# Performance work log

Measured on AMD Instinct MI355X. Metric: run time of the kernel, lower is better.

## Reference

```python
import jax, jax.numpy as jnp
import numpy as np
from jax import lax

MARGIN = 1.0
LAMDA = 0.003
EPS = 1e-9


def extract_features(f, idx):
    # f: (B,C,h,w); idx: (B,N,2) int with idx[...,0]=x, idx[...,1]=y -> (B*N, C)
    B, N = idx.shape[:2]
    b = jnp.arange(B)[:, None]
    x = idx[..., 0]
    y = idx[..., 1]
    g = f[b, :, y, x]  # (B, N, C)
    return g.reshape(B * N, f.shape[1])


def grad_axis(f, axis):
    # np.gradient along one axis: central differences, one-sided at edges
    fl = jnp.moveaxis(f, axis, 0)
    g = jnp.concatenate([
        fl[1:2] - fl[0:1],
        (fl[2:] - fl[:-2]) * 0.5,
        fl[-1:] - fl[-2:-1],
    ], axis=0)
    return jnp.moveaxis(g, 0, axis)


def contrastive(fa, fb, N, pos):
    diff = fa - fb
    if pos:
        return jnp.sum(diff * diff / N)
    m = jnp.maximum(MARGIN - diff, 0.0)
    return jnp.sum(m * m / N)


def gn_loss(f_t, fb, ub):
    # f_t: (B*N, C) target features; fb: (B,C,h,w); ub: (B,N,2) int matches
    B, N = ub.shape[:2]
    xs = ub  # deterministic stand-in for round(rand + ub) rejection sampling
    f_s = extract_features(fb, xs)
    r = f_s - f_t  # (BN, C)
    fbd = lax.stop_gradient(fb)  # original uses fb.detach() for gradients
    gy = grad_axis(fbd, 2)
    gx = grad_axis(fbd, 3)
    Jx = extract_features(gx, xs)  # (BN, C)
    Jy = extract_features(gy, xs)
    J = jnp.stack([Jx, Jy], axis=-1)  # (BN, C, 2)
    H = jnp.einsum('nci,ncj->nij', J, J) + EPS * jnp.eye(2, dtype=fb.dtype)
    b = jnp.einsum('nci,nc->ni', J, r)  # (BN, 2)
    xsf = xs.reshape(B * N, 2).astype(fb.dtype)
    miu = xsf - jnp.einsum('nij,nj->ni', jnp.linalg.inv(H), b)
    d = ub.reshape(B * N, 2).astype(fb.dtype) - miu
    e1 = 0.5 * jnp.sum(jnp.einsum('na,nab,nb->n', d, H, d))
    log_det = jnp.log(jnp.linalg.det(H))
    e2 = B * N * jnp.log(jnp.asarray(2.0 * np.pi, fb.dtype)) - 0.5 * jnp.sum(log_det)
    return e1 + e2


def gn_forward(F_a, F_b, ka, kb, na, nb):
    N = ka.shape[1]
    fa4 = extract_features(F_a[-1], ka)
    fb4 = extract_features(F_b[-1], kb)
    loss = 0.0
    for i in range(4):
        level = 2 ** (3 - i)
        if i == 3:
            fa_pos, fb_pos = fa4, fb4
        else:
            fa_pos = extract_features(F_a[i], ka // level)
            fb_pos = extract_features(F_b[i], kb // level)
        fa_neg = extract_features(F_a[i], na // level)
        fb_neg = extract_features(F_b[i], nb // level)
        loss_pos = contrastive(fa_pos, fb_pos, N, pos=True)
        loss_neg = contrastive(fa_neg, fb_neg, N, pos=False)
        loss_gn = gn_loss(fa_pos, F_b[i], kb // level)
        loss = loss_pos + loss_neg + LAMDA * loss_gn + loss
    return loss


def setup_inputs() -> dict:
    key = jax.random.key(0)
    ks = jax.random.split(key, 12)
    B, C, H, W, N = 4, 64, 256, 256, 512
    inp = {}
    for j, (name, s) in enumerate([
        ('fa0', 32), ('fa1', 64), ('fa2', 128), ('fa3', 256),
        ('fb0', 32), ('fb1', 64), ('fb2', 128), ('fb3', 256)]):
        inp[name] = jax.random.normal(ks[j], (B, C, s, s), dtype=jnp.float32)
    for j, name in enumerate(['ka', 'kb', 'na', 'nb']):
        inp[name] = jax.random.randint(ks[8 + j], (B, N, 2), 0, 256, dtype=jnp.int32)
    return inp


def reference(fa0, fa1, fa2, fa3, fb0, fb1, fb2, fb3, ka, kb, na, nb):
    F_a = [fa0, fa1, fa2, fa3]
    F_b = [fb0, fb1, fb2, fb3]
    return gn_forward(F_a, F_b, ka, kb, na, nb)
```

## Files before the change

### kernel.cpp

```cpp
#include <hip/hip_runtime.h>

#define MARGIN 1.0f
#define LAMDA  0.003f
#define EPS_H  1e-9f

#define E2_CONST (0.003f * 4.0f * 2048.0f * 1.8378770664093453f)

__global__ __launch_bounds__(256) void gn_task_kernel(
    const float* __restrict__ fa0, const float* __restrict__ fa1,
    const float* __restrict__ fa2, const float* __restrict__ fa3,
    const float* __restrict__ fb0, const float* __restrict__ fb1,
    const float* __restrict__ fb2, const float* __restrict__ fb3,
    const int* __restrict__ ka, const int* __restrict__ kb,
    const int* __restrict__ na, const int* __restrict__ nb,
    float* __restrict__ partial)
{
    const int wave = threadIdx.x >> 6;
    const int lane = threadIdx.x & 63;
    const int level = wave;
    const int n     = blockIdx.x;
    const int task  = level * 2048 + n;
    const int b     = n >> 9;
    const int shift = 3 - level;
    const int S     = 32 << level;

    const float* fa; const float* fb;
    switch (level) {
        case 0:  fa = fa0; fb = fb0; break;
        case 1:  fa = fa1; fb = fb1; break;
        case 2:  fa = fa2; fb = fb2; break;
        default: fa = fa3; fb = fb3; break;
    }

    const int pidx = n * 2;
    const int kax = ka[pidx]     >> shift;
    const int kay = ka[pidx + 1] >> shift;
    const int kbx = kb[pidx]     >> shift;
    const int kby = kb[pidx + 1] >> shift;
    const int nax = na[pidx]     >> shift;
    const int nay = na[pidx + 1] >> shift;
    const int nbx = nb[pidx]     >> shift;
    const int nby = nb[pidx + 1] >> shift;

    const int plane = (b * 64 + lane) * (S * S);

    const float va  = fa[plane + kay * S + kax];
    const float vb  = fb[plane + kby * S + kbx];
    const float vna = fa[plane + nay * S + nax];
    const float vnb = fb[plane + nby * S + nbx];

    const int   xm = (kbx > 0)     ? kbx - 1 : 0;
    const int   xp = (kbx < S - 1) ? kbx + 1 : S - 1;
    const float sx = (kbx > 0 && kbx < S - 1) ? 0.5f : 1.0f;
    const float Jx = (fb[plane + kby * S + xp] - fb[plane + kby * S + xm]) * sx;

    const int   ym = (kby > 0)     ? kby - 1 : 0;
    const int   yp = (kby < S - 1) ? kby + 1 : S - 1;
    const float sy = (kby > 0 && kby < S - 1) ? 0.5f : 1.0f;
    const float Jy = (fb[plane + yp * S + kbx] - fb[plane + ym * S + kbx]) * sy;

    const float dpos = va - vb;
    const float dneg = vna - vnb;
    const float mneg = fmaxf(MARGIN - dneg, 0.0f);
    const float r    = vb - va;

    float vals[7];
    vals[0] = dpos * dpos;
    vals[1] = mneg * mneg;
    vals[2] = Jx * Jx;
    vals[3] = Jx * Jy;
    vals[4] = Jy * Jy;
    vals[5] = Jx * r;
    vals[6] = Jy * r;

    #pragma unroll
    for (int mask = 32; mask >= 1; mask >>= 1) {
        #pragma unroll
        for (int t = 0; t < 7; ++t)
            vals[t] += __shfl_xor(vals[t], mask, 64);
    }

    if (lane == 0) {
        const float Hxx = vals[2] + EPS_H;
        const float Hxy = vals[3];
        const float Hyy = vals[4] + EPS_H;
        const float bX  = vals[5];
        const float bY  = vals[6];
        const float det = Hxx * Hyy - Hxy * Hxy;
        const float e1  = 0.5f * (Hyy * bX * bX - 2.0f * Hxy * bX * bY + Hxx * bY * bY) / det;
        const float out = (vals[0] + vals[1]) * (1.0f / 512.0f)
                        + LAMDA * (e1 - 0.5f * logf(det));
        partial[task] = out;
    }
}

__global__ __launch_bounds__(256) void gn_reduce_kernel(
    const float* __restrict__ partial, float* __restrict__ out)
{
    __shared__ float sm[256];
    float s = 0.0f;
    for (int i = threadIdx.x; i < 8192; i += 256)
        s += partial[i];
    sm[threadIdx.x] = s;
    __syncthreads();
    #pragma unroll
    for (int off = 128; off >= 1; off >>= 1) {
        if (threadIdx.x < off)
            sm[threadIdx.x] += sm[threadIdx.x + off];
        __syncthreads();
    }
    if (threadIdx.x == 0)
        out[0] = sm[0] + E2_CONST;
}

extern "C" void kernel_launch(void* const* d_in, const int* in_sizes, int n_in,
                              void* d_out, int out_size, void* d_ws, size_t ws_size,
                              hipStream_t stream) {
    const float* fa0 = (const float*)d_in[0];
    const float* fa1 = (const float*)d_in[1];
    const float* fa2 = (const float*)d_in[2];
    const float* fa3 = (const float*)d_in[3];
    const float* fb0 = (const float*)d_in[4];
    const float* fb1 = (const float*)d_in[5];
    const float* fb2 = (const float*)d_in[6];
    const float* fb3 = (const float*)d_in[7];
    const int*   ka  = (const int*)d_in[8];
    const int*   kb  = (const int*)d_in[9];
    const int*   na  = (const int*)d_in[10];
    const int*   nb  = (const int*)d_in[11];

    float* partial = (float*)d_ws;
    float* out     = (float*)d_out;

    gn_task_kernel<<<2048, 256, 0, stream>>>(fa0, fa1, fa2, fa3,
                                             fb0, fb1, fb2, fb3,
                                             ka, kb, na, nb, partial);
    gn_reduce_kernel<<<1, 256, 0, stream>>>(partial, out);
}
```

Before: 53.68 us.

## Process two points per wave and fuse final reduction via atomics

```diff
diff --git a/kernel.cpp b/kernel.cpp
--- a/kernel.cpp
+++ b/kernel.cpp
@@ -6,6 +6,43 @@
 
 #define E2_CONST (0.003f * 4.0f * 2048.0f * 1.8378770664093453f)
 
+struct PointVals { float v[7]; };
+
+__device__ __forceinline__ void point_addrs(
+    const int* __restrict__ ka, const int* __restrict__ kb,
+    const int* __restrict__ na, const int* __restrict__ nb,
+    int n, int shift, int S, int plane,
+    int& a_pos, int& a_neg_a, int& a_bpos, int& a_neg_b,
+    int& a_xm, int& a_xp, int& a_ym, int& a_yp,
+    float& sx, float& sy)
+{
+    const int2 kA = ((const int2*)ka)[n];
+    const int2 kB = ((const int2*)kb)[n];
+    const int2 nA = ((const int2*)na)[n];
+    const int2 nB = ((const int2*)nb)[n];
+    const int kax = kA.x >> shift, kay = kA.y >> shift;
+    const int kbx = kB.x >> shift, kby = kB.y >> shift;
+    const int nax = nA.x >> shift, nay = nA.y >> shift;
+    const int nbx = nB.x >> shift, nby = nB.y >> shift;
+
+    a_pos   = plane + kay * S + kax;
+    a_neg_a = plane + nay * S + nax;
+    a_bpos  = plane + kby * S + kbx;
+    a_neg_b = plane + nby * S + nbx;
+
+    const int xm = (kbx > 0)     ? kbx - 1 : 0;
+    const int xp = (kbx < S - 1) ? kbx + 1 : S - 1;
+    sx = (kbx > 0 && kbx < S - 1) ? 0.5f : 1.0f;
+    a_xm = plane + kby * S + xm;
+    a_xp = plane + kby * S + xp;
+
+    const int ym = (kby > 0)     ? kby - 1 : 0;
+    const int yp = (kby < S - 1) ? kby + 1 : S - 1;
+    sy = (kby > 0 && kby < S - 1) ? 0.5f : 1.0f;
+    a_ym = plane + ym * S + kbx;
+    a_yp = plane + yp * S + kbx;
+}
+
 __global__ __launch_bounds__(256) void gn_task_kernel(
     const float* __restrict__ fa0, const float* __restrict__ fa1,
     const float* __restrict__ fa2, const float* __restrict__ fa3,
@@ -13,16 +50,19 @@
     const float* __restrict__ fb2, const float* __restrict__ fb3,
     const int* __restrict__ ka, const int* __restrict__ kb,
     const int* __restrict__ na, const int* __restrict__ nb,
-    float* __restrict__ partial)
+    float* __restrict__ out)
 {
+    __shared__ float blk[4];
     const int wave = threadIdx.x >> 6;
     const int lane = threadIdx.x & 63;
     const int level = wave;
-    const int n     = blockIdx.x;
-    const int task  = level * 2048 + n;
-    const int b     = n >> 9;
     const int shift = 3 - level;
     const int S     = 32 << level;
+
+    const int n0 = blockIdx.x;
+    const int n1 = blockIdx.x + 1024;
+    const int b0 = n0 >> 9;
+    const int b1 = n1 >> 9;
 
     const float* fa; const float* fb;
     switch (level) {
@@ -32,85 +72,86 @@
         default: fa = fa3; fb = fb3; break;
     }
 
-    const int pidx = n * 2;
-    const int kax = ka[pidx]     >> shift;
-    const int kay = ka[pidx + 1] >> shift;
-    const int kbx = kb[pidx]     >> shift;
-    const int kby = kb[pidx + 1] >> shift;
-    const int nax = na[pidx]     >> shift;
-    const int nay = na[pidx + 1] >> shift;
-    const int nbx = nb[pidx]     >> shift;
-    const int nby = nb[pidx + 1] >> shift;
+    const int plane0 = (b0 * 64 + lane) * (S * S);
+    const int plane1 = (b1 * 64 + lane) * (S * S);
 
-    const int plane = (b * 64 + lane) * (S * S);
+    int p0_pos, p0_na, p0_bp, p0_nb, p0_xm, p0_xp, p0_ym, p0_yp;
+    int p1_pos, p1_na, p1_bp, p1_nb, p1_xm, p1_xp, p1_ym, p1_yp;
+    float sx0, sy0, sx1, sy1;
+    point_addrs(ka, kb, na, nb, n0, shift, S, plane0,
+                p0_pos, p0_na, p0_bp, p0_nb, p0_xm, p0_xp, p0_ym, p0_yp, sx0, sy0);
+    point_addrs(ka, kb, na, nb, n1, shift, S, plane1,
+                p1_pos, p1_na, p1_bp, p1_nb, p1_xm, p1_xp, p1_ym, p1_yp, sx1, sy1);
 
-    const float va  = fa[plane + kay * S + kax];
-    const float vb  = fb[plane + kby * S + kbx];
-    const float vna = fa[plane + nay * S + nax];
-    const float vnb = fb[plane + nby * S + nbx];
+    const float va0  = fa[p0_pos];
+    const float vna0 = fa[p0_na];
+    const float vb0  = fb[p0_bp];
+    const float vnb0 = fb[p0_nb];
+    const float gxm0 = fb[p0_xm];
+    const float gxp0 = fb[p0_xp];
+    const float gym0 = fb[p0_ym];
+    const float gyp0 = fb[p0_yp];
+    const float va1  = fa[p1_pos];
+    const float vna1 = fa[p1_na];
+    const float vb1  = fb[p1_bp];
+    const float vnb1 = fb[p1_nb];
+    const float gxm1 = fb[p1_xm];
+    const float gxp1 = fb[p1_xp];
+    const float gym1 = fb[p1_ym];
+    const float gyp1 = fb[p1_yp];
 
-    const int   xm = (kbx > 0)     ? kbx - 1 : 0;
-    const int   xp = (kbx < S - 1) ? kbx + 1 : S - 1;
-    const float sx = (kbx > 0 && kbx < S - 1) ? 0.5f : 1.0f;
-    const float Jx = (fb[plane + kby * S + xp] - fb[plane + kby * S + xm]) * sx;
+    const float Jx0 = (gxp0 - gxm0) * sx0;
+    const float Jy0 = (gyp0 - gym0) * sy0;
+    const float Jx1 = (gxp1 - gxm1) * sx1;
+    const float Jy1 = (gyp1 - gym1) * sy1;
 
-    const int   ym = (kby > 0)     ? kby - 1 : 0;
-    const int   yp = (kby < S - 1) ? kby + 1 : S - 1;
-    const float sy = (kby > 0 && kby < S - 1) ? 0.5f : 1.0f;
-    const float Jy = (fb[plane + yp * S + kbx] - fb[plane + ym * S + kbx]) * sy;
+    const float dpos0 = va0 - vb0;
+    const float dneg0 = vna0 - vnb0;
+    const float mneg0 = fmaxf(MARGIN - dneg0, 0.0f);
+    const float r0    = vb0 - va0;
+    const float dpos1 = va1 - vb1;
+    const float dneg1 = vna1 - vnb1;
+    const float mneg1 = fmaxf(MARGIN - dneg1, 0.0f);
+    const float r1    = vb1 - va1;
 
-    const float dpos = va - vb;
-    const float dneg = vna - vnb;
-    const float mneg = fmaxf(MARGIN - dneg, 0.0f);
-    const float r    = vb - va;
-
-    float vals[7];
-    vals[0] = dpos * dpos;
-    vals[1] = mneg * mneg;
-    vals[2] = Jx * Jx;
-    vals[3] = Jx * Jy;
-    vals[4] = Jy * Jy;
-    vals[5] = Jx * r;
-    vals[6] = Jy * r;
+    float vals[14];
+    vals[0]  = dpos0 * dpos0;   vals[7]  = dpos1 * dpos1;
+    vals[1]  = mneg0 * mneg0;   vals[8]  = mneg1 * mneg1;
+    vals[2]  = Jx0 * Jx0;       vals[9]  = Jx1 * Jx1;
+    vals[3]  = Jx0 * Jy0;       vals[10] = Jx1 * Jy1;
+    vals[4]  = Jy0 * Jy0;       vals[11] = Jy1 * Jy1;
+    vals[5]  = Jx0 * r0;        vals[12] = Jx1 * r1;
+    vals[6]  = Jy0 * r0;        vals[13] = Jy1 * r1;
 
     #pragma unroll
     for (int mask = 32; mask >= 1; mask >>= 1) {
         #pragma unroll
-        for (int t = 0; t < 7; ++t)
+        for (int t = 0; t < 14; ++t)
             vals[t] += __shfl_xor(vals[t], mask, 64);
     }
 
     if (lane == 0) {
-        const float Hxx = vals[2] + EPS_H;
-        const float Hxy = vals[3];
-        const float Hyy = vals[4] + EPS_H;
-        const float bX  = vals[5];
-        const float bY  = vals[6];
-        const float det = Hxx * Hyy - Hxy * Hxy;
-        const float e1  = 0.5f * (Hyy * bX * bX - 2.0f * Hxy * bX * bY + Hxx * bY * bY) / det;
-        const float out = (vals[0] + vals[1]) * (1.0f / 512.0f)
-                        + LAMDA * (e1 - 0.5f * logf(det));
-        partial[task] = out;
+        float o = 0.0f;
+        #pragma unroll
+        for (int p = 0; p < 2; ++p) {
+            const float* v = vals + p * 7;
+            const float Hxx = v[2] + EPS_H;
+            const float Hxy = v[3];
+            const float Hyy = v[4] + EPS_H;
+            const float bX  = v[5];
+            const float bY  = v[6];
+            const float det = Hxx * Hyy - Hxy * Hxy;
+            const float e1  = 0.5f * (Hyy * bX * bX - 2.0f * Hxy * bX * bY + Hxx * bY * bY) / det;
+            o += (v[0] + v[1]) * (1.0f / 512.0f) + LAMDA * (e1 - 0.5f * logf(det));
+        }
+        blk[wave] = o;
     }
-}
-
-__global__ __launch_bounds__(256) void gn_reduce_kernel(
-    const float* __restrict__ partial, float* __restrict__ out)
-{
-    __shared__ float sm[256];
-    float s = 0.0f;
-    for (int i = threadIdx.x; i < 8192; i += 256)
-        s += partial[i];
-    sm[threadIdx.x] = s;
     __syncthreads();
-    #pragma unroll
-    for (int off = 128; off >= 1; off >>= 1) {
-        if (threadIdx.x < off)
-            sm[threadIdx.x] += sm[threadIdx.x + off];
-        __syncthreads();
+    if (threadIdx.x == 0) {
+        float s = blk[0] + blk[1] + blk[2] + blk[3];
+        if (blockIdx.x == 0) s += E2_CONST;
+        atomicAdd(out, s);
     }
-    if (threadIdx.x == 0)
-        out[0] = sm[0] + E2_CONST;
 }
 
 extern "C" void kernel_launch(void* const* d_in, const int* in_sizes, int n_in,
@@ -129,11 +170,10 @@
     const int*   na  = (const int*)d_in[10];
     const int*   nb  = (const int*)d_in[11];
 
-    float* partial = (float*)d_ws;
-    float* out     = (float*)d_out;
+    float* out = (float*)d_out;
+    hipMemsetAsync(out, 0, sizeof(float), stream);
 
-    gn_task_kernel<<<2048, 256, 0, stream>>>(fa0, fa1, fa2, fa3,
+    gn_task_kernel<<<1024, 256, 0, stream>>>(fa0, fa1, fa2, fa3,
                                              fb0, fb1, fb2, fb3,
-                                             ka, kb, na, nb, partial);
-    gn_reduce_kernel<<<1, 256, 0, stream>>>(partial, out);
+                                             ka, kb, na, nb, out);
 }
```

After: 59.77 us. 11.4% more time.

## Rebalance level work across waves and fuse final reduction via atomics

Applied to the files above, without the earlier changes.

```diff
diff --git a/kernel.cpp b/kernel.cpp
--- a/kernel.cpp
+++ b/kernel.cpp
@@ -6,6 +6,55 @@
 
 #define E2_CONST (0.003f * 4.0f * 2048.0f * 1.8378770664093453f)
 
+__device__ __forceinline__ float finalize_level(const float* v) {
+    const float Hxx = v[2] + EPS_H;
+    const float Hxy = v[3];
+    const float Hyy = v[4] + EPS_H;
+    const float bX  = v[5];
+    const float bY  = v[6];
+    const float det = Hxx * Hyy - Hxy * Hxy;
+    const float e1  = 0.5f * (Hyy * bX * bX - 2.0f * Hxy * bX * bY + Hxx * bY * bY) / det;
+    return (v[0] + v[1]) * (1.0f / 512.0f) + LAMDA * (e1 - 0.5f * logf(det));
+}
+
+__device__ __forceinline__ void gather7(
+    const float* __restrict__ fa, const float* __restrict__ fb,
+    int2 kA, int2 kB, int2 nA, int2 nB,
+    int shift, int S, int plane, float* v)
+{
+    const int kax = kA.x >> shift, kay = kA.y >> shift;
+    const int kbx = kB.x >> shift, kby = kB.y >> shift;
+    const int nax = nA.x >> shift, nay = nA.y >> shift;
+    const int nbx = nB.x >> shift, nby = nB.y >> shift;
+
+    const float va  = fa[plane + kay * S + kax];
+    const float vna = fa[plane + nay * S + nax];
+    const float vb  = fb[plane + kby * S + kbx];
+    const float vnb = fb[plane + nby * S + nbx];
+
+    const int   xm = (kbx > 0)     ? kbx - 1 : 0;
+    const int   xp = (kbx < S - 1) ? kbx + 1 : S - 1;
+    const float sx = (kbx > 0 && kbx < S - 1) ? 0.5f : 1.0f;
+    const int   ym = (kby > 0)     ? kby - 1 : 0;
+    const int   yp = (kby < S - 1) ? kby + 1 : S - 1;
+    const float sy = (kby > 0 && kby < S - 1) ? 0.5f : 1.0f;
+    const float Jx = (fb[plane + kby * S + xp] - fb[plane + kby * S + xm]) * sx;
+    const float Jy = (fb[plane + yp * S + kbx] - fb[plane + ym * S + kbx]) * sy;
+
+    const float dpos = va - vb;
+    const float dneg = vna - vnb;
+    const float mneg = fmaxf(MARGIN - dneg, 0.0f);
+    const float r    = vb - va;
+
+    v[0] = dpos * dpos;
+    v[1] = mneg * mneg;
+    v[2] = Jx * Jx;
+    v[3] = Jx * Jy;
+    v[4] = Jy * Jy;
+    v[5] = Jx * r;
+    v[6] = Jy * r;
+}
+
 __global__ __launch_bounds__(256) void gn_task_kernel(
     const float* __restrict__ fa0, const float* __restrict__ fa1,
     const float* __restrict__ fa2, const float* __restrict__ fa3,
@@ -13,104 +62,114 @@
     const float* __restrict__ fb2, const float* __restrict__ fb3,
     const int* __restrict__ ka, const int* __restrict__ kb,
     const int* __restrict__ na, const int* __restrict__ nb,
-    float* __restrict__ partial)
+    float* __restrict__ out)
 {
+    __shared__ float l3sums[2][7];
+    __shared__ float wloss[2];
+
     const int wave = threadIdx.x >> 6;
     const int lane = threadIdx.x & 63;
-    const int level = wave;
-    const int n     = blockIdx.x;
-    const int task  = level * 2048 + n;
-    const int b     = n >> 9;
-    const int shift = 3 - level;
-    const int S     = 32 << level;
+    const int n    = blockIdx.x;
+    const int b    = n >> 9;
 
-    const float* fa; const float* fb;
-    switch (level) {
-        case 0:  fa = fa0; fb = fb0; break;
-        case 1:  fa = fa1; fb = fb1; break;
-        case 2:  fa = fa2; fb = fb2; break;
-        default: fa = fa3; fb = fb3; break;
+    const int2 kA = ((const int2*)ka)[n];
+    const int2 kB = ((const int2*)kb)[n];
+    const int2 nA = ((const int2*)na)[n];
+    const int2 nB = ((const int2*)nb)[n];
+
+    if (wave < 2) {
+        const int role = lane >> 5;
+        const int c    = (wave << 5) + (lane & 31);
+        const int plane = (b * 64 + c) * (256 * 256);
+
+        const int a0v = plane + kA.y * 256 + kA.x;
+        const int a1v = plane + nA.y * 256 + nA.x;
+        const int a2v = plane + kB.y * 256 + kB.x;
+        const int a3v = plane + nB.y * 256 + nB.x;
+
+        const int kbx = kB.x, kby = kB.y;
+        const int xm = (kbx > 0)   ? kbx - 1 : 0;
+        const int xp = (kbx < 255) ? kbx + 1 : 255;
+        const float sx = (kbx > 0 && kbx < 255) ? 0.5f : 1.0f;
+        const int ym = (kby > 0)   ? kby - 1 : 0;
+        const int yp = (kby < 255) ? kby + 1 : 255;
+        const float sy = (kby > 0 && kby < 255) ? 0.5f : 1.0f;
+        const int a0g = plane + kby * 256 + xm;
+        const int a1g = plane + kby * 256 + xp;
+        const int a2g = plane + ym * 256 + kbx;
+        const int a3g = plane + yp * 256 + kbx;
+
+        const float* p0 = role ? fb3 : fa3;
+        const float* p1 = role ? fb3 : fa3;
+        const int a0 = role ? a0g : a0v;
+        const int a1 = role ? a1g : a1v;
+        const int a2 = role ? a2g : a2v;
+        const int a3 = role ? a3g : a3v;
+
+        const float L0 = p0[a0];
+        const float L1 = p1[a1];
+        const float L2 = fb3[a2];
+        const float L3 = fb3[a3];
+
+        const float r    = L2 - L0;
+        const float rsw  = __shfl_xor(r, 32, 64);
+        const float Jx   = (L1 - L0) * sx;
+        const float Jy   = (L3 - L2) * sy;
+        const float dpos = L0 - L2;
+        const float dneg = L1 - L3;
+        const float mneg = fmaxf(MARGIN - dneg, 0.0f);
+
+        float v[7];
+        v[0] = role ? 0.0f : dpos * dpos;
+        v[1] = role ? 0.0f : mneg * mneg;
+        v[2] = role ? Jx * Jx  : 0.0f;
+        v[3] = role ? Jx * Jy  : 0.0f;
+        v[4] = role ? Jy * Jy  : 0.0f;
+        v[5] = role ? Jx * rsw : 0.0f;
+        v[6] = role ? Jy * rsw : 0.0f;
+
+        #pragma unroll
+        for (int mask = 32; mask >= 1; mask >>= 1)
+            #pragma unroll
+            for (int t = 0; t < 7; ++t)
+                v[t] += __shfl_xor(v[t], mask, 64);
+
+        if (lane == 0)
+            #pragma unroll
+            for (int t = 0; t < 7; ++t) l3sums[wave][t] = v[t];
+    } else if (wave == 2) {
+        float v[7];
+        const int plane = (b * 64 + lane) * (128 * 128);
+        gather7(fa2, fb2, kA, kB, nA, nB, 1, 128, plane, v);
+        #pragma unroll
+        for (int mask = 32; mask >= 1; mask >>= 1)
+            #pragma unroll
+            for (int t = 0; t < 7; ++t)
+                v[t] += __shfl_xor(v[t], mask, 64);
+        if (lane == 0) wloss[0] = finalize_level(v);
+    } else {
+        float v[14];
+        const int plane1 = (b * 64 + lane) * (64 * 64);
+        const int plane0 = (b * 64 + lane) * (32 * 32);
+        gather7(fa1, fb1, kA, kB, nA, nB, 2, 64, plane1, v);
+        gather7(fa0, fb0, kA, kB, nA, nB, 3, 32, plane0, v + 7);
+        #pragma unroll
+        for (int mask = 32; mask >= 1; mask >>= 1)
+            #pragma unroll
+            for (int t = 0; t < 14; ++t)
+                v[t] += __shfl_xor(v[t], mask, 64);
+        if (lane == 0) wloss[1] = finalize_level(v) + finalize_level(v + 7);
     }
 
-    const int pidx = n * 2;
-    const int kax = ka[pidx]     >> shift;
-    const int kay = ka[pidx + 1] >> shift;
-    const int kbx = kb[pidx]     >> shift;
-    const int kby = kb[pidx + 1] >> shift;
-    const int nax = na[pidx]     >> shift;
-    const int nay = na[pidx + 1] >> shift;
-    const int nbx = nb[pidx]     >> shift;
-    const int nby = nb[pidx + 1] >> shift;
-
-    const int plane = (b * 64 + lane) * (S * S);
-
-    const float va  = fa[plane + kay * S + kax];
-    const float vb  = fb[plane + kby * S + kbx];
-    const float vna = fa[plane + nay * S + nax];
-    const float vnb = fb[plane + nby * S + nbx];
-
-    const int   xm = (kbx > 0)     ? kbx - 1 : 0;
-    const int   xp = (kbx < S - 1) ? kbx + 1 : S - 1;
-    const float sx = (kbx > 0 && kbx < S - 1) ? 0.5f : 1.0f;
-    const float Jx = (fb[plane + kby * S + xp] - fb[plane + kby * S + xm]) * sx;
-
-    const int   ym = (kby > 0)     ? kby - 1 : 0;
-    const int   yp = (kby < S - 1) ? kby + 1 : S - 1;
-    const float sy = (kby > 0 && kby < S - 1) ? 0.5f : 1.0f;
-    const float Jy = (fb[plane + yp * S + kbx] - fb[plane + ym * S + kbx]) * sy;
-
-    const float dpos = va - vb;
-    const float dneg = vna - vnb;
-    const float mneg = fmaxf(MARGIN - dneg, 0.0f);
-    const float r    = vb - va;
-
-    float vals[7];
-    vals[0] = dpos * dpos;
-    vals[1] = mneg * mneg;
-    vals[2] = Jx * Jx;
-    vals[3] = Jx * Jy;
-    vals[4] = Jy * Jy;
-    vals[5] = Jx * r;
-    vals[6] = Jy * r;
-
-    #pragma unroll
-    for (int mask = 32; mask >= 1; mask >>= 1) {
+    __syncthreads();
+    if (threadIdx.x == 0) {
+        float v3[7];
         #pragma unroll
-        for (int t = 0; t < 7; ++t)
-            vals[t] += __shfl_xor(vals[t], mask, 64);
+        for (int t = 0; t < 7; ++t) v3[t] = l3sums[0][t] + l3sums[1][t];
+        float s = finalize_level(v3) + wloss[0] + wloss[1];
+        if (blockIdx.x == 0) s += E2_CONST;
+        atomicAdd(out, s);
     }
-
-    if (lane == 0) {
-        const float Hxx = vals[2] + EPS_H;
-        const float Hxy = vals[3];
-        const float Hyy = vals[4] + EPS_H;
-        const float bX  = vals[5];
-        const float bY  = vals[6];
-        const float det = Hxx * Hyy - Hxy * Hxy;
-        const float e1  = 0.5f * (Hyy * bX * bX - 2.0f * Hxy * bX * bY + Hxx * bY * bY) / det;
-        const float out = (vals[0] + vals[1]) * (1.0f / 512.0f)
-                        + LAMDA * (e1 - 0.5f * logf(det));
-        partial[task] = out;
-    }
-}
-
-__global__ __launch_bounds__(256) void gn_reduce_kernel(
-    const float* __restrict__ partial, float* __restrict__ out)
-{
-    __shared__ float sm[256];
-    float s = 0.0f;
-    for (int i = threadIdx.x; i < 8192; i += 256)
-        s += partial[i];
-    sm[threadIdx.x] = s;
-    __syncthreads();
-    #pragma unroll
-    for (int off = 128; off >= 1; off >>= 1) {
-        if (threadIdx.x < off)
-            sm[threadIdx.x] += sm[threadIdx.x + off];
-        __syncthreads();
-    }
-    if (threadIdx.x == 0)
-        out[0] = sm[0] + E2_CONST;
 }
 
 extern "C" void kernel_launch(void* const* d_in, const int* in_sizes, int n_in,
@@ -129,11 +188,10 @@
     const int*   na  = (const int*)d_in[10];
     const int*   nb  = (const int*)d_in[11];
 
-    float* partial = (float*)d_ws;
-    float* out     = (float*)d_out;
+    float* out = (float*)d_out;
+    hipMemsetAsync(out, 0, sizeof(float), stream);
 
     gn_task_kernel<<<2048, 256, 0, stream>>>(fa0, fa1, fa2, fa3,
                                              fb0, fb1, fb2, fb3,
-                                             ka, kb, na, nb, partial);
-    gn_reduce_kernel<<<1, 256, 0, stream>>>(partial, out);
+                                             ka, kb, na, nb, out);
 }
```

New measurement: 55.57 us. 3.5% more time.
